# Optimization experiments

Measured on AMD Instinct MI355X. Metric: run time of the kernel, lower is better.

The kernel has to match this reference:

```python
import jax, jax.numpy as jnp
import numpy as np

NUM_LAYERS = 2
D = 1024
DIN = 2048
N_STATE = 16
K = 4
EPS = 1e-5


def layer_norm(x, w, b):
    m = jnp.mean(x, axis=-1, keepdims=True)
    v = jnp.mean(jnp.square(x - m), axis=-1, keepdims=True)
    return (x - m) * jax.lax.rsqrt(v + EPS) * w + b


def selective_ssm(x, A_log, Wdt, b_dt, WB, WC, D_skip):
    # x: [B, L, DIN]; diagonal selective SSM (Mamba-style)
    A = -jnp.exp(A_log)                      # [DIN, N]
    dt = jax.nn.softplus(x @ Wdt + b_dt)     # [B, L, DIN]
    Bm = x @ WB                              # [B, L, N]
    Cm = x @ WC                              # [B, L, N]

    def step(h, inp):
        x_t, dt_t, B_t, C_t = inp            # [B,DIN],[B,DIN],[B,N],[B,N]
        dA = jnp.exp(dt_t[..., None] * A)    # [B, DIN, N]
        h = h * dA + (dt_t * x_t)[..., None] * B_t[:, None, :]
        y = jnp.einsum('bdn,bn->bd', h, C_t)
        return h, y

    xs = (x.transpose(1, 0, 2), dt.transpose(1, 0, 2),
          Bm.transpose(1, 0, 2), Cm.transpose(1, 0, 2))
    h0 = jnp.zeros((x.shape[0], x.shape[2], N_STATE), x.dtype)
    h_last, ys = jax.lax.scan(step, h0, xs)
    y = ys.transpose(1, 0, 2) + x * D_skip
    return y, h_last


def causal_dwconv(x, w, b):
    # x: [B, L, DIN]; w: [K, DIN] depthwise causal conv
    xp = jnp.pad(x, ((0, 0), (K - 1, 0), (0, 0)))
    out = jax.lax.conv_general_dilated(
        xp, w[:, None, :], (1,), 'VALID',
        dimension_numbers=('NWC', 'WIO', 'NWC'),
        feature_group_count=x.shape[-1])
    return out + b


def setup_inputs() -> dict:
    key = jax.random.key(0)
    ks = jax.random.split(key, 12)
    s = 0.02
    B, L = 2, 2048
    return {
        'x': jax.random.normal(ks[0], (B, L, D), jnp.float32),
        'pos_emb': jax.random.normal(ks[1], (L, D), jnp.float32) * s,
        'norm_w': jnp.ones((NUM_LAYERS, D), jnp.float32),
        'norm_b': jnp.zeros((NUM_LAYERS, D), jnp.float32),
        'Win': jax.random.normal(ks[2], (NUM_LAYERS, D, DIN), jnp.float32) * s,
        'b_in': jnp.zeros((NUM_LAYERS, DIN), jnp.float32),
        'A_log': jax.random.uniform(ks[3], (NUM_LAYERS, DIN, N_STATE), jnp.float32),
        'Wdt': jax.random.normal(ks[4], (NUM_LAYERS, DIN, DIN), jnp.float32) * s,
        'b_dt': jax.random.normal(ks[5], (NUM_LAYERS, DIN), jnp.float32) - 4.0,
        'WB': jax.random.normal(ks[6], (NUM_LAYERS, DIN, N_STATE), jnp.float32) * s,
        'WC': jax.random.normal(ks[7], (NUM_LAYERS, DIN, N_STATE), jnp.float32) * s,
        'D_skip': jnp.ones((NUM_LAYERS, DIN), jnp.float32),
        'conv_w': jax.random.normal(ks[8], (NUM_LAYERS, K, DIN), jnp.float32) * s,
        'conv_b': jnp.zeros((NUM_LAYERS, DIN), jnp.float32),
        'Wout': jax.random.normal(ks[9], (NUM_LAYERS, DIN, D), jnp.float32) * s,
        'b_out': jnp.zeros((NUM_LAYERS, D), jnp.float32),
        'fnorm_w': jnp.ones((D,), jnp.float32),
        'fnorm_b': jnp.zeros((D,), jnp.float32),
    }


def reference(x, pos_emb, norm_w, norm_b, Win, b_in, A_log, Wdt, b_dt, WB, WC,
              D_skip, conv_w, conv_b, Wout, b_out, fnorm_w, fnorm_b):
    L = x.shape[1]
    x = x + pos_emb[:L]
    for i in range(NUM_LAYERS):
        res = x
        h = layer_norm(x, norm_w[i], norm_b[i])
        h = h @ Win[i] + b_in[i]                       # [B, L, DIN]
        y_ssm, _ = selective_ssm(h, A_log[i], Wdt[i], b_dt[i], WB[i], WC[i], D_skip[i])
        y_conv = jax.nn.silu(causal_dwconv(h, conv_w[i], conv_b[i]))
        g = y_ssm * jax.nn.sigmoid(y_conv)             # gating
        x = g @ Wout[i] + b_out[i] + res               # dropout is identity (eval)
    return layer_norm(x, fnorm_w, fnorm_b)
```

## Files before the change

### kernel.cpp

```cpp
#include <hip/hip_runtime.h>
#include <cstdint>
#include <cstddef>

#define D_MODEL 1024
#define DIN     2048
#define NSTATE  16
#define LSEQ    2048
#define NBATCH  2
#define NROWS   (NBATCH*LSEQ)
#define NCOL    (DIN + 128)
#define CCH     64
#define TC      (LSEQ/CCH)

typedef float  f32x4  __attribute__((ext_vector_type(4)));
typedef short  bf16x8 __attribute__((ext_vector_type(8)));
typedef unsigned short us8 __attribute__((ext_vector_type(8)));

__device__ __forceinline__ unsigned short f2bf(float f) {
  union { float f; unsigned u; } c; c.f = f;
  unsigned x = c.u + 0x7fffu + ((c.u >> 16) & 1u);
  return (unsigned short)(x >> 16);
}
__device__ __forceinline__ float bf2f(unsigned short u) {
  union { unsigned u; float f; } c; c.u = (unsigned)u << 16; return c.f;
}
__device__ __forceinline__ float sigmoidf_(float x) {
  return __builtin_amdgcn_rcpf(1.f + __expf(-x));
}
__device__ __forceinline__ float softplusf_(float x) {
  return fmaxf(x, 0.f) + __logf(1.f + __expf(-fabsf(x)));
}

__device__ __forceinline__ void gll16(const void* g, void* l) {
  __builtin_amdgcn_global_load_lds(
      (const __attribute__((address_space(1))) void*)g,
      (__attribute__((address_space(3))) void*)l, 16, 0, 0);
}

__global__ __launch_bounds__(256) void ln_kernel(const float* __restrict__ Xin,
    const float* __restrict__ pos, const unsigned short* __restrict__ P, int nP,
    const float* __restrict__ bex, const float* __restrict__ w,
    const float* __restrict__ b, unsigned short* __restrict__ outB,
    float* __restrict__ outF, float* __restrict__ Xw) {
  const int row = blockIdx.x, t = threadIdx.x;
  float4 v = *(const float4*)(Xin + (size_t)row * D_MODEL + t * 4);
  if (pos) {
    const float4 p = *(const float4*)(pos + (size_t)(row & (LSEQ - 1)) * D_MODEL + t * 4);
    v.x += p.x; v.y += p.y; v.z += p.z; v.w += p.w;
  }
  if (P) {
    const size_t MN = (size_t)NROWS * D_MODEL;
    const size_t e = (size_t)row * D_MODEL + t * 4;
    float a0 = 0.f, a1 = 0.f, a2 = 0.f, a3 = 0.f;
#pragma unroll 2
    for (int k = 0; k < nP; k++) {
      const ushort4 u = *(const ushort4*)(P + k * MN + e);
      a0 += bf2f(u.x); a1 += bf2f(u.y); a2 += bf2f(u.z); a3 += bf2f(u.w);
    }
    const float4 be = *(const float4*)(bex + t * 4);
    v.x += a0 + be.x; v.y += a1 + be.y; v.z += a2 + be.z; v.w += a3 + be.w;
  }
  if (Xw) *(float4*)(Xw + (size_t)row * D_MODEL + t * 4) = v;
  float s  = v.x + v.y + v.z + v.w;
  float s2 = v.x * v.x + v.y * v.y + v.z * v.z + v.w * v.w;
#pragma unroll
  for (int o = 1; o < 64; o <<= 1) { s += __shfl_xor(s, o, 64); s2 += __shfl_xor(s2, o, 64); }
  __shared__ float ps[8];
  int wv = t >> 6;
  if ((t & 63) == 0) { ps[wv] = s; ps[wv + 4] = s2; }
  __syncthreads();
  s  = ps[0] + ps[1] + ps[2] + ps[3];
  s2 = ps[4] + ps[5] + ps[6] + ps[7];
  float mean = s * (1.f / D_MODEL);
  float var  = s2 * (1.f / D_MODEL) - mean * mean;
  float rs   = rsqrtf(var + 1e-5f);
  const float4 wv4 = *(const float4*)(w + t * 4);
  const float4 bv4 = *(const float4*)(b + t * 4);
  float o0 = (v.x - mean) * rs * wv4.x + bv4.x;
  float o1 = (v.y - mean) * rs * wv4.y + bv4.y;
  float o2 = (v.z - mean) * rs * wv4.z + bv4.z;
  float o3 = (v.w - mean) * rs * wv4.w + bv4.w;
  if (outB) {
    ushort4 o; o.x = f2bf(o0); o.y = f2bf(o1); o.z = f2bf(o2); o.w = f2bf(o3);
    *(ushort4*)(outB + (size_t)row * D_MODEL + t * 4) = o;
  } else {
    float4 o; o.x = o0; o.y = o1; o.z = o2; o.w = o3;
    *(float4*)(outF + (size_t)row * D_MODEL + t * 4) = o;
  }
}

__global__ __launch_bounds__(256) void tcvt_kernel(const float* __restrict__ in0,
    unsigned short* __restrict__ out0, int K_, int N_,
    size_t inLS, size_t outLS) {
  const float* in = in0 + (size_t)blockIdx.z * inLS;
  unsigned short* out = out0 + (size_t)blockIdx.z * outLS;
  __shared__ float tile[64][68];
  int n0 = blockIdx.x * 64, k0 = blockIdx.y * 64;
  int t = threadIdx.x;
  int r = t >> 4, cc = (t & 15) * 4;
#pragma unroll
  for (int j = 0; j < 4; j++) {
    const float4 v = *(const float4*)(in + (size_t)(k0 + r + j * 16) * N_ + n0 + cc);
    tile[r + j * 16][cc + 0] = v.x; tile[r + j * 16][cc + 1] = v.y;
    tile[r + j * 16][cc + 2] = v.z; tile[r + j * 16][cc + 3] = v.w;
  }
  __syncthreads();
  int nr = t >> 2, kc = (t & 3) * 16;
  unsigned u[8];
#pragma unroll
  for (int i = 0; i < 8; i++) {
    unsigned lo = f2bf(tile[kc + 2 * i][nr]);
    unsigned hi = f2bf(tile[kc + 2 * i + 1][nr]);
    u[i] = lo | (hi << 16);
  }
  uint4* dst = (uint4*)(out + (size_t)(n0 + nr) * K_ + k0 + kc);
  uint4 w0; w0.x = u[0]; w0.y = u[1]; w0.z = u[2]; w0.w = u[3];
  uint4 w1; w1.x = u[4]; w1.y = u[5]; w1.z = u[6]; w1.w = u[7];
  dst[0] = w0; dst[1] = w1;
}

__global__ __launch_bounds__(256) void wprep_kernel(const float* __restrict__ WB0,
    const float* __restrict__ WC0, const float* __restrict__ b_dt0,
    unsigned short* __restrict__ Wt0, float* __restrict__ bias20) {
  const int L = blockIdx.y;
  const float* WB = WB0 + (size_t)L * DIN * NSTATE;
  const float* WC = WC0 + (size_t)L * DIN * NSTATE;
  const float* b_dt = b_dt0 + (size_t)L * DIN;
  unsigned short* Wt = Wt0 + (size_t)L * NCOL * DIN;
  float* bias2 = bias20 + (size_t)L * NCOL;
  int id = blockIdx.x * 256 + threadIdx.x;
  if (id < 65536) {
    int k = id & (DIN - 1);
    int n2 = id >> 11;
    float v = (n2 < NSTATE) ? WB[(size_t)k * NSTATE + n2]
                            : WC[(size_t)k * NSTATE + (n2 - NSTATE)];
    Wt[(size_t)(DIN + n2) * DIN + k] = f2bf(v);
  } else if (id < 90112) {
    int z = id - 65536;
    uint4 zz; zz.x = zz.y = zz.z = zz.w = 0u;
    *(uint4*)(Wt + (size_t)2080 * DIN + (size_t)z * 8) = zz;
  } else if (id < 90112 + NCOL) {
    int i = id - 90112;
    bias2[i] = (i < DIN) ? b_dt[i] : 0.f;
  }
}

__global__ __launch_bounds__(256) void gemm_kernel(
    const unsigned short* __restrict__ A, const unsigned short* __restrict__ Bt,
    const float* __restrict__ bias, unsigned short* __restrict__ outP,
    int M, int N, int Kfull, int kLen) {
  __shared__ unsigned short smem[6 * 128 * 32];
  unsigned short* sA = smem;
  unsigned short* sB = smem + 3 * 4096;
  const int t = threadIdx.x;
  const int lane = t & 63, wave = t >> 6;
  const int wr = wave >> 1, wc = wave & 1;

  const int gx = gridDim.x, gy = gridDim.y;
  const int orig = (blockIdx.z * gy + blockIdx.y) * gx + blockIdx.x;
  const int nwg = gx * gy * gridDim.z;
  const int q = nwg >> 3, r = nwg & 7;
  const int xcd = orig & 7, pp = orig >> 3;
  const int wgid = (xcd < r) ? (xcd * (q + 1) + pp)
                             : (r * (q + 1) + (xcd - r) * q + pp);
  const int nt = wgid % gx;
  const int mt = (wgid / gx) % gy;
  const int ks = wgid / (gx * gy);
  const int m0 = mt * 128, n0 = nt * 128;

  const int ar = t >> 2;
  const int acs = (((t & 3) ^ ((ar >> 1) & 3)) << 3);
  const int wseg = wave * 16 * 32;
  const int lr = lane & 15;
  const int swA = (((lane >> 4) ^ ((lr >> 1) & 3)) << 3);

  f32x4 acc[4][4];
#pragma unroll
  for (int m = 0; m < 4; m++)
#pragma unroll
    for (int n = 0; n < 4; n++) acc[m][n] = (f32x4)0.f;

  const int kBeg = ks * kLen;
  const int NT = kLen >> 5;

  auto STAGE = [&](int bi, int k0) {
    gll16(A  + (size_t)(m0 + ar) * Kfull + k0 + acs,      &sA[bi * 4096 + wseg]);
    gll16(A  + (size_t)(m0 + 64 + ar) * Kfull + k0 + acs, &sA[bi * 4096 + 64 * 32 + wseg]);
    gll16(Bt + (size_t)(n0 + ar) * Kfull + k0 + acs,      &sB[bi * 4096 + wseg]);
    gll16(Bt + (size_t)(n0 + 64 + ar) * Kfull + k0 + acs, &sB[bi * 4096 + 64 * 32 + wseg]);
  };
  auto COMPUTE = [&](int bi) {
    bf16x8 af[4], bg[4];
#pragma unroll
    for (int m = 0; m < 4; m++)
      af[m] = *(const bf16x8*)(&sA[bi * 4096 + (wr * 64 + m * 16 + lr) * 32 + swA]);
#pragma unroll
    for (int n = 0; n < 4; n++)
      bg[n] = *(const bf16x8*)(&sB[bi * 4096 + (wc * 64 + n * 16 + lr) * 32 + swA]);
#pragma unroll
    for (int m = 0; m < 4; m++)
#pragma unroll
      for (int n = 0; n < 4; n++)
        acc[m][n] = __builtin_amdgcn_mfma_f32_16x16x32_bf16(af[m], bg[n], acc[m][n], 0, 0, 0);
  };

  STAGE(0, kBeg); STAGE(1, kBeg + 32);
  for (int tt = 0; tt < NT - 1; ++tt) {
    asm volatile("s_waitcnt vmcnt(4)" ::: "memory");
    __builtin_amdgcn_s_barrier();
    if (tt + 2 < NT) STAGE((tt + 2) % 3, kBeg + ((tt + 2) << 5));
    COMPUTE(tt % 3);
  }
  asm volatile("s_waitcnt vmcnt(0)" ::: "memory");
  __builtin_amdgcn_s_barrier();
  COMPUTE((NT - 1) % 3);

  __syncthreads();
  unsigned short* sC = smem + wave * 4096;
  const int lq = lane >> 4;
#pragma unroll
  for (int m = 0; m < 4; m++)
#pragma unroll
    for (int n = 0; n < 4; n++) {
      const int lcol = n * 16 + lr;
      const int col = n0 + wc * 64 + lcol;
      const float bv = (bias && ks == 0) ? bias[col] : 0.f;
#pragma unroll
      for (int j = 0; j < 4; j++) {
        const int lrow = m * 16 + lq * 4 + j;
        const int sc = lcol ^ (((lrow >> 2) & 3) << 4);
        sC[lrow * 64 + sc] = f2bf(acc[m][n][j] + bv);
      }
    }
  unsigned short* out = outP + (size_t)ks * M * N;
  const int rowbase = m0 + wr * 64, colbase = n0 + wc * 64;
  const int rr = lane >> 3, ch = lane & 7;
#pragma unroll
  for (int i = 0; i < 8; i++) {
    const int row = i * 8 + rr;
    const int sb = (ch * 16) ^ (((row >> 2) & 3) << 5);
    us8 v = *(const us8*)((const char*)sC + row * 128 + sb);
    *(us8*)(out + (size_t)(rowbase + row) * N + colbase + ch * 8) = v;
  }
}

__global__ __launch_bounds__(256) void scan1_kernel(
    const unsigned short* __restrict__ DTP, const unsigned short* __restrict__ Hbf,
    const float* __restrict__ A_log, float* __restrict__ Hc, float* __restrict__ Pc) {
  const unsigned short* DT1 = DTP + (size_t)NROWS * NCOL;
  const int tid = threadIdx.x;
  const int d0 = blockIdx.x * 256, d = d0 + tid;
  const int b = blockIdx.y, c = blockIdx.z;
  __shared__ unsigned short ssp[TC][256];
  __shared__ unsigned short sxx[TC][256];
  __shared__ float sBC[TC][32];
  const size_t base = (size_t)b * LSEQ + c * TC;
#pragma unroll
  for (int it = 0; it < TC * 32 / 256; ++it) {
    int idx = it * 256 + tid;
    int tt = idx >> 5, cc = (idx & 31) * 8;
    us8 a = *(const us8*)(DTP + (base + tt) * NCOL + d0 + cc);
    us8 bb = *(const us8*)(DT1 + (base + tt) * NCOL + d0 + cc);
    us8 o;
#pragma unroll
    for (int j = 0; j < 8; j++) o[j] = f2bf(softplusf_(bf2f(a[j]) + bf2f(bb[j])));
    *(us8*)&ssp[tt][cc] = o;
    *(us8*)&sxx[tt][cc] = *(const us8*)(Hbf + (base + tt) * DIN + d0 + cc);
  }
  if (tid < TC * 4) {
    int tt = tid >> 2, cc = (tid & 3) * 8;
    us8 v0 = *(const us8*)(DTP + (base + tt) * NCOL + DIN + cc);
    us8 v1 = *(const us8*)(DT1 + (base + tt) * NCOL + DIN + cc);
#pragma unroll
    for (int j = 0; j < 8; j++) sBC[tt][cc + j] = bf2f(v0[j]) + bf2f(v1[j]);
  }
  float a2[16], h[16];
#pragma unroll
  for (int n = 0; n < 16; n++) {
    a2[n] = -__expf(A_log[(size_t)d * NSTATE + n]);
    h[n] = 0.f;
  }
  __syncthreads();
  float S = 0.f;
  for (int tt = 0; tt < TC; ++tt) {
    float sp = bf2f(ssp[tt][tid]);
    float x  = bf2f(sxx[tt][tid]);
    S += sp;
    float sx = sp * x;
#pragma unroll
    for (int n = 0; n < 16; n++)
      h[n] = fmaf(h[n], __expf(sp * a2[n]), sx * sBC[tt][n]);
  }
  const size_t chain = ((size_t)c * (NBATCH * DIN) + (size_t)b * DIN + d) * 16;
#pragma unroll
  for (int n = 0; n < 16; n++) {
    Hc[chain + n] = h[n];
    Pc[chain + n] = __expf(S * a2[n]);
  }
}

__global__ __launch_bounds__(256) void scomb_kernel(float* __restrict__ Hc,
    const float* __restrict__ Pc) {
  const size_t id = (size_t)blockIdx.x * 256 + threadIdx.x;
  const size_t stride = (size_t)NBATCH * DIN * NSTATE;
  float h = 0.f;
  for (int c = 0; c < CCH; c++) {
    size_t o = (size_t)c * stride + id;
    float hl = Hc[o], p = Pc[o];
    Hc[o] = h;
    h = fmaf(p, h, hl);
  }
}

__global__ __launch_bounds__(256) void scan2g_kernel(
    const unsigned short* __restrict__ DTP, const unsigned short* __restrict__ Hbf,
    const float* __restrict__ A_log, const float* __restrict__ Hinit,
    const float* __restrict__ cw, const float* __restrict__ cb,
    const float* __restrict__ dsk, unsigned short* __restrict__ G) {
  const unsigned short* DT1 = DTP + (size_t)NROWS * NCOL;
  const int tid = threadIdx.x;
  const int d0 = blockIdx.x * 256, d = d0 + tid;
  const int b = blockIdx.y, c = blockIdx.z;
  __shared__ unsigned short ssp[TC][256];
  __shared__ unsigned short sxx[TC][256];
  __shared__ float sBC[TC][32];
  const size_t base = (size_t)b * LSEQ + c * TC;
#pragma unroll
  for (int it = 0; it < TC * 32 / 256; ++it) {
    int idx = it * 256 + tid;
    int tt = idx >> 5, cc = (idx & 31) * 8;
    us8 a = *(const us8*)(DTP + (base + tt) * NCOL + d0 + cc);
    us8 bb = *(const us8*)(DT1 + (base + tt) * NCOL + d0 + cc);
    us8 o;
#pragma unroll
    for (int j = 0; j < 8; j++) o[j] = f2bf(softplusf_(bf2f(a[j]) + bf2f(bb[j])));
    *(us8*)&ssp[tt][cc] = o;
    *(us8*)&sxx[tt][cc] = *(const us8*)(Hbf + (base + tt) * DIN + d0 + cc);
  }
  if (tid < TC * 4) {
    int tt = tid >> 2, cc = (tid & 3) * 8;
    us8 v0 = *(const us8*)(DTP + (base + tt) * NCOL + DIN + cc);
    us8 v1 = *(const us8*)(DT1 + (base + tt) * NCOL + DIN + cc);
#pragma unroll
    for (int j = 0; j < 8; j++) sBC[tt][cc + j] = bf2f(v0[j]) + bf2f(v1[j]);
  }
  const size_t chain = ((size_t)c * (NBATCH * DIN) + (size_t)b * DIN + d) * 16;
  float a2[16], h[16];
#pragma unroll
  for (int n = 0; n < 16; n++) {
    a2[n] = -__expf(A_log[(size_t)d * NSTATE + n]);
    h[n] = Hinit[chain + n];
  }
  const float w0 = cw[d], w1 = cw[DIN + d], w2 = cw[2 * DIN + d], w3 = cw[3 * DIN + d];
  const float cbv = cb[d], dsv = dsk[d];
  const int t0 = c * TC;
  float xm1 = (t0 >= 1) ? bf2f(Hbf[(base - 1) * DIN + d]) : 0.f;
  float xm2 = (t0 >= 2) ? bf2f(Hbf[(base - 2) * DIN + d]) : 0.f;
  float xm3 = (t0 >= 3) ? bf2f(Hbf[(base - 3) * DIN + d]) : 0.f;
  __syncthreads();
  for (int tt = 0; tt < TC; ++tt) {
    float sp = bf2f(ssp[tt][tid]);
    float x  = bf2f(sxx[tt][tid]);
    float sx = sp * x;
    float y0 = 0.f, y1 = 0.f, y2 = 0.f, y3 = 0.f;
#pragma unroll
    for (int n = 0; n < 16; n += 4) {
      h[n]     = fmaf(h[n],     __expf(sp * a2[n]),     sx * sBC[tt][n]);
      h[n + 1] = fmaf(h[n + 1], __expf(sp * a2[n + 1]), sx * sBC[tt][n + 1]);
      h[n + 2] = fmaf(h[n + 2], __expf(sp * a2[n + 2]), sx * sBC[tt][n + 2]);
      h[n + 3] = fmaf(h[n + 3], __expf(sp * a2[n + 3]), sx * sBC[tt][n + 3]);
      y0 = fmaf(h[n],     sBC[tt][16 + n],     y0);
      y1 = fmaf(h[n + 1], sBC[tt][16 + n + 1], y1);
      y2 = fmaf(h[n + 2], sBC[tt][16 + n + 2], y2);
      y3 = fmaf(h[n + 3], sBC[tt][16 + n + 3], y3);
    }
    float y = (y0 + y1) + (y2 + y3);
    float a = cbv + w0 * xm3 + w1 * xm2 + w2 * xm1 + w3 * x;
    float sl = a * sigmoidf_(a);
    float g = (y + x * dsv) * sigmoidf_(sl);
    G[(base + tt) * DIN + d] = f2bf(g);
    xm3 = xm2; xm2 = xm1; xm1 = x;
  }
}

extern "C" void kernel_launch(void* const* d_in, const int* in_sizes, int n_in,
                              void* d_out, int out_size, void* d_ws, size_t ws_size,
                              hipStream_t stream) {
  const float* x_in   = (const float*)d_in[0];
  const float* pos    = (const float*)d_in[1];
  const float* norm_w = (const float*)d_in[2];
  const float* norm_b = (const float*)d_in[3];
  const float* Win    = (const float*)d_in[4];
  const float* b_in   = (const float*)d_in[5];
  const float* A_log  = (const float*)d_in[6];
  const float* Wdt    = (const float*)d_in[7];
  const float* b_dt   = (const float*)d_in[8];
  const float* WB     = (const float*)d_in[9];
  const float* WC     = (const float*)d_in[10];
  const float* Dsk    = (const float*)d_in[11];
  const float* conv_w = (const float*)d_in[12];
  const float* conv_b = (const float*)d_in[13];
  const float* Wout   = (const float*)d_in[14];
  const float* b_out  = (const float*)d_in[15];
  const float* fnw    = (const float*)d_in[16];
  const float* fnb    = (const float*)d_in[17];

  uint8_t* ws = (uint8_t*)d_ws;
  constexpr size_t OFF_X     = 0;
  constexpr size_t OFF_HBF   = 16777216;
  constexpr size_t OFF_DT    = 33554432;
  constexpr size_t OFF_XG    = 69206016;
  constexpr size_t OFF_HC    = 85983232;
  constexpr size_t OFF_PC    = 102760448;
  constexpr size_t OFF_WINT  = 119537664;
  constexpr size_t OFF_WDT   = 127926272;
  constexpr size_t OFF_WOUT  = 145752064;
  constexpr size_t OFF_BIAS2 = 154140672;
  constexpr size_t WS_NEEDED = 154158080;
  if (ws_size < WS_NEEDED) return;

  float* X             = (float*)(ws + OFF_X);
  unsigned short* Hbf  = (unsigned short*)(ws + OFF_HBF);
  unsigned short* DTP  = (unsigned short*)(ws + OFF_DT);
  unsigned short* WoutP= (unsigned short*)(ws + OFF_DT);
  unsigned short* Xn   = (unsigned short*)(ws + OFF_XG);
  unsigned short* Gb   = (unsigned short*)(ws + OFF_XG);
  float* Hc            = (float*)(ws + OFF_HC);
  float* Pc            = (float*)(ws + OFF_PC);
  unsigned short* WinT   = (unsigned short*)(ws + OFF_WINT);
  unsigned short* WdtBCT = (unsigned short*)(ws + OFF_WDT);
  unsigned short* WoutT  = (unsigned short*)(ws + OFF_WOUT);
  float* bias2         = (float*)(ws + OFF_BIAS2);

  tcvt_kernel<<<dim3(32, 16, 2), 256, 0, stream>>>(
      Win, WinT, 1024, 2048, (size_t)D_MODEL * DIN, (size_t)DIN * D_MODEL);
  tcvt_kernel<<<dim3(32, 32, 2), 256, 0, stream>>>(
      Wdt, WdtBCT, 2048, 2048, (size_t)DIN * DIN, (size_t)NCOL * DIN);
  tcvt_kernel<<<dim3(16, 32, 2), 256, 0, stream>>>(
      Wout, WoutT, 2048, 1024, (size_t)DIN * D_MODEL, (size_t)D_MODEL * DIN);
  wprep_kernel<<<dim3(361, 2), 256, 0, stream>>>(WB, WC, b_dt, WdtBCT, bias2);

  for (int i = 0; i < 2; i++) {
    unsigned short* WinT_i   = WinT + (size_t)i * DIN * D_MODEL;
    unsigned short* WdtBCT_i = WdtBCT + (size_t)i * NCOL * DIN;
    unsigned short* WoutT_i  = WoutT + (size_t)i * D_MODEL * DIN;
    float* bias2_i           = bias2 + (size_t)i * NCOL;

    if (i == 0)
      ln_kernel<<<4096, 256, 0, stream>>>(x_in, pos, nullptr, 0, nullptr,
                                          norm_w, norm_b, Xn, nullptr, X);
    else
      ln_kernel<<<4096, 256, 0, stream>>>(X, nullptr, WoutP, 2, b_out,
                                          norm_w + D_MODEL, norm_b + D_MODEL,
                                          Xn, nullptr, X);
    gemm_kernel<<<dim3(16, 32, 1), 256, 0, stream>>>(
        Xn, WinT_i, b_in + (size_t)i * DIN, Hbf, NROWS, DIN, D_MODEL, 1024);
    gemm_kernel<<<dim3(17, 32, 2), 256, 0, stream>>>(
        Hbf, WdtBCT_i, bias2_i, DTP, NROWS, NCOL, DIN, 1024);
    scan1_kernel<<<dim3(DIN / 256, NBATCH, CCH), 256, 0, stream>>>(
        DTP, Hbf, A_log + (size_t)i * DIN * NSTATE, Hc, Pc);
    scomb_kernel<<<(NBATCH * DIN * NSTATE) / 256, 256, 0, stream>>>(Hc, Pc);
    scan2g_kernel<<<dim3(DIN / 256, NBATCH, CCH), 256, 0, stream>>>(
        DTP, Hbf, A_log + (size_t)i * DIN * NSTATE, Hc,
        conv_w + (size_t)i * 4 * DIN, conv_b + (size_t)i * DIN,
        Dsk + (size_t)i * DIN, Gb);
    gemm_kernel<<<dim3(8, 32, 2), 256, 0, stream>>>(
        Gb, WoutT_i, nullptr, WoutP, NROWS, D_MODEL, DIN, 1024);
  }

  ln_kernel<<<4096, 256, 0, stream>>>(X, nullptr, WoutP, 2, b_out + D_MODEL,
                                      fnw, fnb, nullptr, (float*)d_out, nullptr);
}
```

Baseline: 434.8 us.

## Fuse chunked scan passes into one cooperative kernel with grid syncs

Replaces the three-kernel chunked selective scan (per-chunk scan, cross-chunk combine, second scan with gating) with one cooperative kernel that uses grid-wide syncs between phases. The softplus(dt), x and B/C values are staged in shared memory once and reused by both scan passes instead of being reloaded from global memory, and two launches go away. In exchange the whole grid (1024 blocks) must be co-resident, and the combine phase runs on only 256 blocks while the rest wait at the barrier. A three-kernel fallback is kept for when occupancy is too low.

```diff
diff --git a/kernel.cpp b/kernel.cpp
--- a/kernel.cpp
+++ b/kernel.cpp
@@ -1,4 +1,5 @@
 #include <hip/hip_runtime.h>
+#include <hip/hip_cooperative_groups.h>
 #include <cstdint>
 #include <cstddef>
 
@@ -11,6 +12,8 @@
 #define NCOL    (DIN + 128)
 #define CCH     64
 #define TC      (LSEQ/CCH)
+
+namespace cg = cooperative_groups;
 
 typedef float  f32x4  __attribute__((ext_vector_type(4)));
 typedef short  bf16x8 __attribute__((ext_vector_type(8)));
@@ -244,6 +247,111 @@
   }
 }
 
+__global__ __launch_bounds__(256) void scanfused_kernel(
+    const unsigned short* __restrict__ DTP, const unsigned short* __restrict__ Hbf,
+    const float* __restrict__ A_log, float* __restrict__ Hc, float* __restrict__ Pc,
+    const float* __restrict__ cw, const float* __restrict__ cb,
+    const float* __restrict__ dsk, unsigned short* __restrict__ G) {
+  const unsigned short* DT1 = DTP + (size_t)NROWS * NCOL;
+  const int tid = threadIdx.x;
+  const int d0 = blockIdx.x * 256, d = d0 + tid;
+  const int b = blockIdx.y, c = blockIdx.z;
+  __shared__ unsigned short ssp[TC][256];
+  __shared__ unsigned short sxx[TC][256];
+  __shared__ float sBC[TC][32];
+  const size_t base = (size_t)b * LSEQ + c * TC;
+#pragma unroll
+  for (int it = 0; it < TC * 32 / 256; ++it) {
+    int idx = it * 256 + tid;
+    int tt = idx >> 5, cc = (idx & 31) * 8;
+    us8 a = *(const us8*)(DTP + (base + tt) * NCOL + d0 + cc);
+    us8 bb = *(const us8*)(DT1 + (base + tt) * NCOL + d0 + cc);
+    us8 o;
+#pragma unroll
+    for (int j = 0; j < 8; j++) o[j] = f2bf(softplusf_(bf2f(a[j]) + bf2f(bb[j])));
+    *(us8*)&ssp[tt][cc] = o;
+    *(us8*)&sxx[tt][cc] = *(const us8*)(Hbf + (base + tt) * DIN + d0 + cc);
+  }
+  if (tid < TC * 4) {
+    int tt = tid >> 2, cc = (tid & 3) * 8;
+    us8 v0 = *(const us8*)(DTP + (base + tt) * NCOL + DIN + cc);
+    us8 v1 = *(const us8*)(DT1 + (base + tt) * NCOL + DIN + cc);
+#pragma unroll
+    for (int j = 0; j < 8; j++) sBC[tt][cc + j] = bf2f(v0[j]) + bf2f(v1[j]);
+  }
+  float a2[16], h[16];
+#pragma unroll
+  for (int n = 0; n < 16; n++) {
+    a2[n] = -__expf(A_log[(size_t)d * NSTATE + n]);
+    h[n] = 0.f;
+  }
+  const int t0 = c * TC;
+  float xm1 = (t0 >= 1) ? bf2f(Hbf[(base - 1) * DIN + d]) : 0.f;
+  float xm2 = (t0 >= 2) ? bf2f(Hbf[(base - 2) * DIN + d]) : 0.f;
+  float xm3 = (t0 >= 3) ? bf2f(Hbf[(base - 3) * DIN + d]) : 0.f;
+  const float w0 = cw[d], w1 = cw[DIN + d], w2 = cw[2 * DIN + d], w3 = cw[3 * DIN + d];
+  const float cbv = cb[d], dsv = dsk[d];
+  __syncthreads();
+
+  float S = 0.f;
+  for (int tt = 0; tt < TC; ++tt) {
+    float sp = bf2f(ssp[tt][tid]);
+    float x  = bf2f(sxx[tt][tid]);
+    S += sp;
+    float sx = sp * x;
+#pragma unroll
+    for (int n = 0; n < 16; n++)
+      h[n] = fmaf(h[n], __expf(sp * a2[n]), sx * sBC[tt][n]);
+  }
+  const size_t chain = ((size_t)c * (NBATCH * DIN) + (size_t)b * DIN + d) * 16;
+#pragma unroll
+  for (int n = 0; n < 16; n++) {
+    Hc[chain + n] = h[n];
+    Pc[chain + n] = __expf(S * a2[n]);
+  }
+  cg::this_grid().sync();
+
+  const int rank = (blockIdx.z * gridDim.y + blockIdx.y) * gridDim.x + blockIdx.x;
+  if (rank < 256) {
+    const size_t id = (size_t)rank * 256 + tid;
+    const size_t stride = (size_t)NBATCH * DIN * NSTATE;
+    float hh = 0.f;
+    for (int cc2 = 0; cc2 < CCH; cc2++) {
+      size_t o = (size_t)cc2 * stride + id;
+      float hl = Hc[o], p = Pc[o];
+      Hc[o] = hh;
+      hh = fmaf(p, hh, hl);
+    }
+  }
+  cg::this_grid().sync();
+
+#pragma unroll
+  for (int n = 0; n < 16; n++) h[n] = Hc[chain + n];
+  for (int tt = 0; tt < TC; ++tt) {
+    float sp = bf2f(ssp[tt][tid]);
+    float x  = bf2f(sxx[tt][tid]);
+    float sx = sp * x;
+    float y0 = 0.f, y1 = 0.f, y2 = 0.f, y3 = 0.f;
+#pragma unroll
+    for (int n = 0; n < 16; n += 4) {
+      h[n]     = fmaf(h[n],     __expf(sp * a2[n]),     sx * sBC[tt][n]);
+      h[n + 1] = fmaf(h[n + 1], __expf(sp * a2[n + 1]), sx * sBC[tt][n + 1]);
+      h[n + 2] = fmaf(h[n + 2], __expf(sp * a2[n + 2]), sx * sBC[tt][n + 2]);
+      h[n + 3] = fmaf(h[n + 3], __expf(sp * a2[n + 3]), sx * sBC[tt][n + 3]);
+      y0 = fmaf(h[n],     sBC[tt][16 + n],     y0);
+      y1 = fmaf(h[n + 1], sBC[tt][16 + n + 1], y1);
+      y2 = fmaf(h[n + 2], sBC[tt][16 + n + 2], y2);
+      y3 = fmaf(h[n + 3], sBC[tt][16 + n + 3], y3);
+    }
+    float y = (y0 + y1) + (y2 + y3);
+    float a = cbv + w0 * xm3 + w1 * xm2 + w2 * xm1 + w3 * x;
+    float sl = a * sigmoidf_(a);
+    float g = (y + x * dsv) * sigmoidf_(sl);
+    G[(base + tt) * DIN + d] = f2bf(g);
+    xm3 = xm2; xm2 = xm1; xm1 = x;
+  }
+}
+
 __global__ __launch_bounds__(256) void scan1_kernel(
     const unsigned short* __restrict__ DTP, const unsigned short* __restrict__ Hbf,
     const float* __restrict__ A_log, float* __restrict__ Hc, float* __restrict__ Pc) {
@@ -432,6 +540,11 @@
   unsigned short* WoutT  = (unsigned short*)(ws + OFF_WOUT);
   float* bias2         = (float*)(ws + OFF_BIAS2);
 
+  int maxB = 0, coopOK = 0;
+  if (hipOccupancyMaxActiveBlocksPerMultiprocessor(
+          &maxB, (const void*)scanfused_kernel, 256, 0) == hipSuccess && maxB >= 4)
+    coopOK = 1;
+
   tcvt_kernel<<<dim3(32, 16, 2), 256, 0, stream>>>(
       Win, WinT, 1024, 2048, (size_t)D_MODEL * DIN, (size_t)DIN * D_MODEL);
   tcvt_kernel<<<dim3(32, 32, 2), 256, 0, stream>>>(
@@ -445,6 +558,10 @@
     unsigned short* WdtBCT_i = WdtBCT + (size_t)i * NCOL * DIN;
     unsigned short* WoutT_i  = WoutT + (size_t)i * D_MODEL * DIN;
     float* bias2_i           = bias2 + (size_t)i * NCOL;
+    const float* alog_i = A_log + (size_t)i * DIN * NSTATE;
+    const float* cw_i   = conv_w + (size_t)i * 4 * DIN;
+    const float* cb_i   = conv_b + (size_t)i * DIN;
+    const float* ds_i   = Dsk + (size_t)i * DIN;
 
     if (i == 0)
       ln_kernel<<<4096, 256, 0, stream>>>(x_in, pos, nullptr, 0, nullptr,
@@ -457,13 +574,23 @@
         Xn, WinT_i, b_in + (size_t)i * DIN, Hbf, NROWS, DIN, D_MODEL, 1024);
     gemm_kernel<<<dim3(17, 32, 2), 256, 0, stream>>>(
         Hbf, WdtBCT_i, bias2_i, DTP, NROWS, NCOL, DIN, 1024);
-    scan1_kernel<<<dim3(DIN / 256, NBATCH, CCH), 256, 0, stream>>>(
-        DTP, Hbf, A_log + (size_t)i * DIN * NSTATE, Hc, Pc);
-    scomb_kernel<<<(NBATCH * DIN * NSTATE) / 256, 256, 0, stream>>>(Hc, Pc);
-    scan2g_kernel<<<dim3(DIN / 256, NBATCH, CCH), 256, 0, stream>>>(
-        DTP, Hbf, A_log + (size_t)i * DIN * NSTATE, Hc,
-        conv_w + (size_t)i * 4 * DIN, conv_b + (size_t)i * DIN,
-        Dsk + (size_t)i * DIN, Gb);
+    if (coopOK) {
+      const unsigned short* DTPc = DTP;
+      const unsigned short* Hbfc = Hbf;
+      unsigned short* Gc = Gb;
+      void* args[] = {(void*)&DTPc, (void*)&Hbfc, (void*)&alog_i, (void*)&Hc,
+                      (void*)&Pc, (void*)&cw_i, (void*)&cb_i, (void*)&ds_i,
+                      (void*)&Gc};
+      hipLaunchCooperativeKernel((const void*)scanfused_kernel,
+                                 dim3(DIN / 256, NBATCH, CCH), dim3(256),
+                                 args, 0, stream);
+    } else {
+      scan1_kernel<<<dim3(DIN / 256, NBATCH, CCH), 256, 0, stream>>>(
+          DTP, Hbf, alog_i, Hc, Pc);
+      scomb_kernel<<<(NBATCH * DIN * NSTATE) / 256, 256, 0, stream>>>(Hc, Pc);
+      scan2g_kernel<<<dim3(DIN / 256, NBATCH, CCH), 256, 0, stream>>>(
+          DTP, Hbf, alog_i, Hc, cw_i, cb_i, ds_i, Gb);
+    }
     gemm_kernel<<<dim3(8, 32, 2), 256, 0, stream>>>(
         Gb, WoutT_i, nullptr, WoutP, NROWS, D_MODEL, DIN, 1024);
   }
```

Result: no change. 434.5 us (-0.1%).

## Stream scan inputs from global with register prefetch instead of shared staging

Applied to the files above, without the earlier changes.

Both scan kernels stop staging softplus(dt) and x for the whole chunk into shared memory. Each thread now loads its own per-timestep bf16 values straight from global memory, prefetching two timesteps ahead in registers, and computes softplus inline in fp32. This removes the shared-memory prologue and the bf16 rounding of dt, and lowers LDS use, which may raise occupancy. In exchange the loads become scalar 2-byte accesses (coalesced across the warp) and softplus is computed per thread.

```diff
diff --git a/kernel.cpp b/kernel.cpp
--- a/kernel.cpp
+++ b/kernel.cpp
@@ -251,22 +251,8 @@
   const int tid = threadIdx.x;
   const int d0 = blockIdx.x * 256, d = d0 + tid;
   const int b = blockIdx.y, c = blockIdx.z;
-  __shared__ unsigned short ssp[TC][256];
-  __shared__ unsigned short sxx[TC][256];
   __shared__ float sBC[TC][32];
   const size_t base = (size_t)b * LSEQ + c * TC;
-#pragma unroll
-  for (int it = 0; it < TC * 32 / 256; ++it) {
-    int idx = it * 256 + tid;
-    int tt = idx >> 5, cc = (idx & 31) * 8;
-    us8 a = *(const us8*)(DTP + (base + tt) * NCOL + d0 + cc);
-    us8 bb = *(const us8*)(DT1 + (base + tt) * NCOL + d0 + cc);
-    us8 o;
-#pragma unroll
-    for (int j = 0; j < 8; j++) o[j] = f2bf(softplusf_(bf2f(a[j]) + bf2f(bb[j])));
-    *(us8*)&ssp[tt][cc] = o;
-    *(us8*)&sxx[tt][cc] = *(const us8*)(Hbf + (base + tt) * DIN + d0 + cc);
-  }
   if (tid < TC * 4) {
     int tt = tid >> 2, cc = (tid & 3) * 8;
     us8 v0 = *(const us8*)(DTP + (base + tt) * NCOL + DIN + cc);
@@ -280,16 +266,32 @@
     a2[n] = -__expf(A_log[(size_t)d * NSTATE + n]);
     h[n] = 0.f;
   }
+  const unsigned short* p0 = DTP + base * NCOL + d;
+  const unsigned short* p1 = DT1 + base * NCOL + d;
+  const unsigned short* px = Hbf + base * DIN + d;
+  unsigned short ua0 = p0[0], ub0 = p1[0], ux0 = px[0];
+  unsigned short ua1 = p0[NCOL], ub1 = p1[NCOL], ux1 = px[DIN];
   __syncthreads();
   float S = 0.f;
-  for (int tt = 0; tt < TC; ++tt) {
-    float sp = bf2f(ssp[tt][tid]);
-    float x  = bf2f(sxx[tt][tid]);
+  for (int tt = 0; tt < TC; tt += 2) {
+    unsigned short na0 = 0, nb0 = 0, nx0 = 0, na1 = 0, nb1 = 0, nx1 = 0;
+    if (tt + 2 < TC) {
+      na0 = p0[(tt + 2) * NCOL]; nb0 = p1[(tt + 2) * NCOL]; nx0 = px[(tt + 2) * DIN];
+      na1 = p0[(tt + 3) * NCOL]; nb1 = p1[(tt + 3) * NCOL]; nx1 = px[(tt + 3) * DIN];
+    }
+    float sp = softplusf_(bf2f(ua0) + bf2f(ub0));
+    float sx = sp * bf2f(ux0);
     S += sp;
-    float sx = sp * x;
 #pragma unroll
     for (int n = 0; n < 16; n++)
       h[n] = fmaf(h[n], __expf(sp * a2[n]), sx * sBC[tt][n]);
+    sp = softplusf_(bf2f(ua1) + bf2f(ub1));
+    sx = sp * bf2f(ux1);
+    S += sp;
+#pragma unroll
+    for (int n = 0; n < 16; n++)
+      h[n] = fmaf(h[n], __expf(sp * a2[n]), sx * sBC[tt + 1][n]);
+    ua0 = na0; ub0 = nb0; ux0 = nx0; ua1 = na1; ub1 = nb1; ux1 = nx1;
   }
   const size_t chain = ((size_t)c * (NBATCH * DIN) + (size_t)b * DIN + d) * 16;
 #pragma unroll
@@ -321,22 +323,8 @@
   const int tid = threadIdx.x;
   const int d0 = blockIdx.x * 256, d = d0 + tid;
   const int b = blockIdx.y, c = blockIdx.z;
-  __shared__ unsigned short ssp[TC][256];
-  __shared__ unsigned short sxx[TC][256];
   __shared__ float sBC[TC][32];
   const size_t base = (size_t)b * LSEQ + c * TC;
-#pragma unroll
-  for (int it = 0; it < TC * 32 / 256; ++it) {
-    int idx = it * 256 + tid;
-    int tt = idx >> 5, cc = (idx & 31) * 8;
-    us8 a = *(const us8*)(DTP + (base + tt) * NCOL + d0 + cc);
-    us8 bb = *(const us8*)(DT1 + (base + tt) * NCOL + d0 + cc);
-    us8 o;
-#pragma unroll
-    for (int j = 0; j < 8; j++) o[j] = f2bf(softplusf_(bf2f(a[j]) + bf2f(bb[j])));
-    *(us8*)&ssp[tt][cc] = o;
-    *(us8*)&sxx[tt][cc] = *(const us8*)(Hbf + (base + tt) * DIN + d0 + cc);
-  }
   if (tid < TC * 4) {
     int tt = tid >> 2, cc = (tid & 3) * 8;
     us8 v0 = *(const us8*)(DTP + (base + tt) * NCOL + DIN + cc);
@@ -357,29 +345,44 @@
   float xm1 = (t0 >= 1) ? bf2f(Hbf[(base - 1) * DIN + d]) : 0.f;
   float xm2 = (t0 >= 2) ? bf2f(Hbf[(base - 2) * DIN + d]) : 0.f;
   float xm3 = (t0 >= 3) ? bf2f(Hbf[(base - 3) * DIN + d]) : 0.f;
+  const unsigned short* p0 = DTP + base * NCOL + d;
+  const unsigned short* p1 = DT1 + base * NCOL + d;
+  const unsigned short* px = Hbf + base * DIN + d;
+  unsigned short ua0 = p0[0], ub0 = p1[0], ux0 = px[0];
+  unsigned short ua1 = p0[NCOL], ub1 = p1[NCOL], ux1 = px[DIN];
   __syncthreads();
-  for (int tt = 0; tt < TC; ++tt) {
-    float sp = bf2f(ssp[tt][tid]);
-    float x  = bf2f(sxx[tt][tid]);
-    float sx = sp * x;
-    float y0 = 0.f, y1 = 0.f, y2 = 0.f, y3 = 0.f;
-#pragma unroll
-    for (int n = 0; n < 16; n += 4) {
-      h[n]     = fmaf(h[n],     __expf(sp * a2[n]),     sx * sBC[tt][n]);
-      h[n + 1] = fmaf(h[n + 1], __expf(sp * a2[n + 1]), sx * sBC[tt][n + 1]);
-      h[n + 2] = fmaf(h[n + 2], __expf(sp * a2[n + 2]), sx * sBC[tt][n + 2]);
-      h[n + 3] = fmaf(h[n + 3], __expf(sp * a2[n + 3]), sx * sBC[tt][n + 3]);
-      y0 = fmaf(h[n],     sBC[tt][16 + n],     y0);
-      y1 = fmaf(h[n + 1], sBC[tt][16 + n + 1], y1);
-      y2 = fmaf(h[n + 2], sBC[tt][16 + n + 2], y2);
-      y3 = fmaf(h[n + 3], sBC[tt][16 + n + 3], y3);
+  for (int tt = 0; tt < TC; tt += 2) {
+    unsigned short na0 = 0, nb0 = 0, nx0 = 0, na1 = 0, nb1 = 0, nx1 = 0;
+    if (tt + 2 < TC) {
+      na0 = p0[(tt + 2) * NCOL]; nb0 = p1[(tt + 2) * NCOL]; nx0 = px[(tt + 2) * DIN];
+      na1 = p0[(tt + 3) * NCOL]; nb1 = p1[(tt + 3) * NCOL]; nx1 = px[(tt + 3) * DIN];
     }
-    float y = (y0 + y1) + (y2 + y3);
-    float a = cbv + w0 * xm3 + w1 * xm2 + w2 * xm1 + w3 * x;
-    float sl = a * sigmoidf_(a);
-    float g = (y + x * dsv) * sigmoidf_(sl);
-    G[(base + tt) * DIN + d] = f2bf(g);
-    xm3 = xm2; xm2 = xm1; xm1 = x;
+#pragma unroll
+    for (int half = 0; half < 2; half++) {
+      const int ts = tt + half;
+      float sp = softplusf_(bf2f(half ? ua1 : ua0) + bf2f(half ? ub1 : ub0));
+      float x  = bf2f(half ? ux1 : ux0);
+      float sx = sp * x;
+      float y0 = 0.f, y1 = 0.f, y2 = 0.f, y3 = 0.f;
+#pragma unroll
+      for (int n = 0; n < 16; n += 4) {
+        h[n]     = fmaf(h[n],     __expf(sp * a2[n]),     sx * sBC[ts][n]);
+        h[n + 1] = fmaf(h[n + 1], __expf(sp * a2[n + 1]), sx * sBC[ts][n + 1]);
+        h[n + 2] = fmaf(h[n + 2], __expf(sp * a2[n + 2]), sx * sBC[ts][n + 2]);
+        h[n + 3] = fmaf(h[n + 3], __expf(sp * a2[n + 3]), sx * sBC[ts][n + 3]);
+        y0 = fmaf(h[n],     sBC[ts][16 + n],     y0);
+        y1 = fmaf(h[n + 1], sBC[ts][16 + n + 1], y1);
+        y2 = fmaf(h[n + 2], sBC[ts][16 + n + 2], y2);
+        y3 = fmaf(h[n + 3], sBC[ts][16 + n + 3], y3);
+      }
+      float y = (y0 + y1) + (y2 + y3);
+      float a = cbv + w0 * xm3 + w1 * xm2 + w2 * xm1 + w3 * x;
+      float sl = a * sigmoidf_(a);
+      float g = (y + x * dsv) * sigmoidf_(sl);
+      G[(base + ts) * DIN + d] = f2bf(g);
+      xm3 = xm2; xm2 = xm1; xm1 = x;
+    }
+    ua0 = na0; ub0 = nb0; ux0 = nx0; ua1 = na1; ub1 = nb1; ux1 = nx1;
   }
 }
 
@@ -445,6 +448,7 @@
     unsigned short* WdtBCT_i = WdtBCT + (size_t)i * NCOL * DIN;
     unsigned short* WoutT_i  = WoutT + (size_t)i * D_MODEL * DIN;
     float* bias2_i           = bias2 + (size_t)i * NCOL;
+    const float* alog_i = A_log + (size_t)i * DIN * NSTATE;
 
     if (i == 0)
       ln_kernel<<<4096, 256, 0, stream>>>(x_in, pos, nullptr, 0, nullptr,
@@ -458,10 +462,10 @@
     gemm_kernel<<<dim3(17, 32, 2), 256, 0, stream>>>(
         Hbf, WdtBCT_i, bias2_i, DTP, NROWS, NCOL, DIN, 1024);
     scan1_kernel<<<dim3(DIN / 256, NBATCH, CCH), 256, 0, stream>>>(
-        DTP, Hbf, A_log + (size_t)i * DIN * NSTATE, Hc, Pc);
+        DTP, Hbf, alog_i, Hc, Pc);
     scomb_kernel<<<(NBATCH * DIN * NSTATE) / 256, 256, 0, stream>>>(Hc, Pc);
     scan2g_kernel<<<dim3(DIN / 256, NBATCH, CCH), 256, 0, stream>>>(
-        DTP, Hbf, A_log + (size_t)i * DIN * NSTATE, Hc,
+        DTP, Hbf, alog_i, Hc,
         conv_w + (size_t)i * 4 * DIN, conv_b + (size_t)i * DIN,
         Dsk + (size_t)i * DIN, Gb);
     gemm_kernel<<<dim3(8, 32, 2), 256, 0, stream>>>(
```

Result: slower. 444.4 us (+2.2%).
